# Performance work log

Measured on AMD Instinct MI355X. Metric: run time of the kernel, lower is better.

## Reference

```python
import jax, jax.numpy as jnp
import numpy as np

KTAPS = 10  # kernel_size in StructuredStateSpace.compute_cauchy_kernel


def setup_inputs() -> dict:
    key = jax.random.key(0)
    ks = jax.random.split(key, 6)
    T, B, F, L, OUT = 8192, 16, 32, 16, 128
    return {
        "x": jax.random.normal(ks[0], (T, B, F), dtype=jnp.float32),
        # K[l, s] = C_l @ A_l^s @ B_l, each an (F, F) matrix (in_features == hidden_size)
        "K": jax.random.normal(ks[1], (L, KTAPS, F, F), dtype=jnp.float32),
        # emission_layer[l]: nn.Linear(hidden_size, 1) -> weight (F,), bias scalar per l
        "em_w": jax.random.normal(ks[2], (L, F), dtype=jnp.float32),
        "em_b": jax.random.normal(ks[3], (L,), dtype=jnp.float32),
        # linear_decoder: nn.Linear(L, out_features)
        "dec_w": jax.random.normal(ks[4], (OUT, L), dtype=jnp.float32),
        "dec_b": jax.random.normal(ks[5], (OUT,), dtype=jnp.float32),
    }


def reference(x, K, em_w, em_b, dec_w, dec_b):
    # x: (T, B, F); K: (L, KTAPS, F, F)
    T, B, F = x.shape
    # causal conv: y[l, t] = sum_{s=0}^{min(t, KTAPS-1)} K[l, s] @ x[t - s]
    xp = jnp.pad(x, ((KTAPS - 1, 0), (0, 0), (0, 0)))  # (T+9, B, F)
    # X[s, t] = x[t - s]  -> (KTAPS, T, B, F); loop is over the fixed 10 taps only
    X = jnp.stack([xp[KTAPS - 1 - s:KTAPS - 1 - s + T] for s in range(KTAPS)], axis=0)
    y = jnp.einsum('lsof,stbf->ltbo', K, X)  # (L, T, B, F)
    # per-branch emission Linear(F, 1), stacked over L -> (T, B, L)
    h = jnp.einsum('ltbo,lo->tbl', y, em_w) + em_b
    h = jnp.swapaxes(h, 0, 1)  # (B, T, L)
    # linear_decoder: (B, T, L) -> (B, T, out_features)
    return h @ dec_w.T + dec_b
```

## Files before the change

### kernel.cpp

```cpp
#include <hip/hip_runtime.h>
#include <hip/hip_bf16.h>

typedef __attribute__((ext_vector_type(4))) float f32x4;
typedef __attribute__((ext_vector_type(8))) short bf16x8;

#define T_DIM 8192
#define B_DIM 16
#define F_DIM 32
#define L_DIM 16
#define NTAPS 10
#define O_DIM 128
#define M_TOTAL (T_DIM * B_DIM)

static __device__ __forceinline__ unsigned short f2bf(float f) {
    union { float f; unsigned int u; } v; v.f = f;
    unsigned int r = v.u + 0x7fffu + ((v.u >> 16) & 1u);
    return (unsigned short)(r >> 16);
}

__global__ __launch_bounds__(256) void build_w2_kernel(
    const float* __restrict__ K, const float* __restrict__ em_w,
    const float* __restrict__ em_b, const float* __restrict__ dec_w,
    const float* __restrict__ dec_b, unsigned short* __restrict__ w2f,
    float* __restrict__ bias2)
{
    int s    = blockIdx.x >> 3;
    int nt   = blockIdx.x & 7;
    int lg   = threadIdx.x >> 6;
    int lane = threadIdx.x & 63;
    int o     = nt * 16 + (lane & 15);
    int fbase = (lane >> 4) * 8;

    float acc[8] = {0.f,0.f,0.f,0.f,0.f,0.f,0.f,0.f};
    for (int l = lg * 4; l < lg * 4 + 4; ++l) {
        float dw = dec_w[o * L_DIM + l];
        const float* Kb = K + (size_t)(l * NTAPS + s) * F_DIM * F_DIM;
        for (int op = 0; op < F_DIM; ++op) {
            float e = em_w[l * F_DIM + op] * dw;
            const float* Kr = Kb + op * F_DIM + fbase;
            #pragma unroll
            for (int j = 0; j < 8; ++j) acc[j] += e * Kr[j];
        }
    }

    __shared__ float red[4][64][8];
    #pragma unroll
    for (int j = 0; j < 8; ++j) red[lg][lane][j] = acc[j];
    __syncthreads();

    if (lg == 0) {
        unsigned short out8[8];
        #pragma unroll
        for (int j = 0; j < 8; ++j) {
            float v = red[0][lane][j] + red[1][lane][j] +
                      red[2][lane][j] + red[3][lane][j];
            out8[j] = f2bf(v);
        }
        unsigned short* dst = w2f + ((size_t)(s * 8 + nt) * 64 + lane) * 8;
        *(bf16x8*)dst = *(const bf16x8*)out8;

        if (s == 0 && lane < 16) {
            int oo = nt * 16 + lane;
            float bsum = dec_b[oo];
            for (int l = 0; l < L_DIM; ++l) bsum += dec_w[oo * L_DIM + l] * em_b[l];
            bias2[oo] = bsum;
        }
    }
}

__global__ __launch_bounds__(256) void convert_x_kernel(
    const float* __restrict__ x, unsigned short* __restrict__ xb)
{
    size_t i = ((size_t)blockIdx.x * 256 + threadIdx.x) * 8;
    f32x4 a = *(const f32x4*)(x + i);
    f32x4 b = *(const f32x4*)(x + i + 4);
    unsigned short r[8];
    #pragma unroll
    for (int j = 0; j < 4; ++j) r[j]     = f2bf(a[j]);
    #pragma unroll
    for (int j = 0; j < 4; ++j) r[4 + j] = f2bf(b[j]);
    *(bf16x8*)(xb + i) = *(const bf16x8*)r;
}

__global__ __launch_bounds__(256) void s4_main_kernel(
    const unsigned short* __restrict__ xb,
    const unsigned short* __restrict__ w2f,
    const float* __restrict__ bias2,
    float* __restrict__ out)
{
    int wave = threadIdx.x >> 6;
    int lane = threadIdx.x & 63;
    int row0 = (blockIdx.x * 4 + wave) * 32;

    f32x4 acc[2][8];
    #pragma unroll
    for (int mt = 0; mt < 2; ++mt)
        #pragma unroll
        for (int nt = 0; nt < 8; ++nt)
            acc[mt][nt] = (f32x4){0.f, 0.f, 0.f, 0.f};

    int lrow = lane & 15;
    int fofs = (lane >> 4) * 8;

    for (int s = 0; s < NTAPS; ++s) {
        bf16x8 bfrag[8];
        const bf16x8* wp = (const bf16x8*)w2f + (size_t)(s * 8) * 64 + lane;
        #pragma unroll
        for (int nt = 0; nt < 8; ++nt) bfrag[nt] = wp[nt * 64];

        #pragma unroll
        for (int mt = 0; mt < 2; ++mt) {
            int r0 = row0 + mt * 16 - s * 16;
            if (r0 >= 0) {
                bf16x8 afrag = *(const bf16x8*)(xb + (size_t)(r0 + lrow) * F_DIM + fofs);
                #pragma unroll
                for (int nt = 0; nt < 8; ++nt)
                    acc[mt][nt] = __builtin_amdgcn_mfma_f32_16x16x32_bf16(
                        afrag, bfrag[nt], acc[mt][nt], 0, 0, 0);
            }
        }
    }

    int og = lane & 15;
    int rg = (lane >> 4) * 4;
    #pragma unroll
    for (int mt = 0; mt < 2; ++mt) {
        #pragma unroll
        for (int nt = 0; nt < 8; ++nt) {
            int o = nt * 16 + og;
            float bo = bias2[o];
            #pragma unroll
            for (int j = 0; j < 4; ++j) {
                int r = row0 + mt * 16 + rg + j;
                int t = r >> 4;
                int b = r & 15;
                out[((size_t)b * T_DIM + t) * O_DIM + o] = acc[mt][nt][j] + bo;
            }
        }
    }
}

extern "C" void kernel_launch(void* const* d_in, const int* in_sizes, int n_in,
                              void* d_out, int out_size, void* d_ws, size_t ws_size,
                              hipStream_t stream)
{
    const float* x     = (const float*)d_in[0];
    const float* K     = (const float*)d_in[1];
    const float* em_w  = (const float*)d_in[2];
    const float* em_b  = (const float*)d_in[3];
    const float* dec_w = (const float*)d_in[4];
    const float* dec_b = (const float*)d_in[5];
    float* out = (float*)d_out;

    const size_t xb_bytes  = (size_t)M_TOTAL * F_DIM * 2;
    const size_t w2f_bytes = (size_t)NTAPS * 8 * 64 * 8 * 2;
    unsigned short* xb  = (unsigned short*)d_ws;
    unsigned short* w2f = (unsigned short*)((char*)d_ws + xb_bytes);
    float* bias2 = (float*)((char*)d_ws + xb_bytes + w2f_bytes);

    hipLaunchKernelGGL(build_w2_kernel, dim3(80), dim3(256), 0, stream,
                       K, em_w, em_b, dec_w, dec_b, w2f, bias2);
    hipLaunchKernelGGL(convert_x_kernel, dim3(M_TOTAL * F_DIM / (256 * 8)), dim3(256), 0, stream,
                       x, xb);
    hipLaunchKernelGGL(s4_main_kernel, dim3(M_TOTAL / 128), dim3(256), 0, stream,
                       xb, w2f, bias2, out);
}
```

Baseline: 129.6 us.

## Transpose x to batch-major padded layout and vectorize output stores

The conversion kernel now writes x in a (B, T+16, F) bf16 layout with zero padding in front. The main kernel can then process contiguous time rows per batch and drop the causal-boundary branch. MFMA operands are swapped so each lane holds four consecutive output columns, which enables 16-byte coalesced float4 stores in the (B,T,O) output order instead of scattered scalar stores. The weight-folding kernel is restructured to first reduce em_w against K in LDS and then apply dec_w, using 10 blocks instead of 80. The costs are a strided read in the transpose kernel and lower parallelism in the small prep kernel.

```diff
diff --git a/kernel.cpp b/kernel.cpp
--- a/kernel.cpp
+++ b/kernel.cpp
@@ -11,6 +11,7 @@
 #define NTAPS 10
 #define O_DIM 128
 #define M_TOTAL (T_DIM * B_DIM)
+#define PADT (T_DIM + 16)
 
 static __device__ __forceinline__ unsigned short f2bf(float f) {
     union { float f; unsigned int u; } v; v.f = f;
@@ -24,62 +25,83 @@
     const float* __restrict__ dec_b, unsigned short* __restrict__ w2f,
     float* __restrict__ bias2)
 {
-    int s    = blockIdx.x >> 3;
-    int nt   = blockIdx.x & 7;
-    int lg   = threadIdx.x >> 6;
-    int lane = threadIdx.x & 63;
-    int o     = nt * 16 + (lane & 15);
-    int fbase = (lane >> 4) * 8;
+    int s = blockIdx.x;
+    int tid = threadIdx.x;
 
-    float acc[8] = {0.f,0.f,0.f,0.f,0.f,0.f,0.f,0.f};
-    for (int l = lg * 4; l < lg * 4 + 4; ++l) {
-        float dw = dec_w[o * L_DIM + l];
-        const float* Kb = K + (size_t)(l * NTAPS + s) * F_DIM * F_DIM;
-        for (int op = 0; op < F_DIM; ++op) {
-            float e = em_w[l * F_DIM + op] * dw;
-            const float* Kr = Kb + op * F_DIM + fbase;
+    __shared__ float Klds[16 * 1024];
+    __shared__ float Glds[16 * 32];
+
+    #pragma unroll
+    for (int l = 0; l < 16; ++l) {
+        const float* src = K + (size_t)(l * NTAPS + s) * 1024 + tid * 4;
+        *(f32x4*)(Klds + l * 1024 + tid * 4) = *(const f32x4*)src;
+    }
+    __syncthreads();
+
+    #pragma unroll
+    for (int rep = 0; rep < 2; ++rep) {
+        int idx = rep * 256 + tid;
+        int l = idx >> 5, f = idx & 31;
+        const float* em = em_w + l * 32;
+        const float* kb = Klds + l * 1024 + f;
+        float g = 0.f;
+        #pragma unroll
+        for (int op = 0; op < 32; ++op) g += em[op] * kb[op * 32];
+        Glds[idx] = g;
+    }
+    __syncthreads();
+
+    int lane = tid & 63;
+    int w    = tid >> 6;
+    int lo   = lane & 15;
+    int fb   = (lane >> 4) * 8;
+    #pragma unroll
+    for (int h = 0; h < 2; ++h) {
+        int nt = w + h * 4;
+        int o  = nt * 16 + lo;
+        float acc[8] = {0.f,0.f,0.f,0.f,0.f,0.f,0.f,0.f};
+        for (int l = 0; l < 16; ++l) {
+            float dw = dec_w[o * L_DIM + l];
+            const float* g = Glds + l * 32 + fb;
             #pragma unroll
-            for (int j = 0; j < 8; ++j) acc[j] += e * Kr[j];
+            for (int j = 0; j < 8; ++j) acc[j] += dw * g[j];
         }
+        unsigned short o8[8];
+        #pragma unroll
+        for (int j = 0; j < 8; ++j) o8[j] = f2bf(acc[j]);
+        *(bf16x8*)(w2f + ((size_t)(s * 8 + nt) * 64 + lane) * 8) = *(const bf16x8*)o8;
     }
 
-    __shared__ float red[4][64][8];
-    #pragma unroll
-    for (int j = 0; j < 8; ++j) red[lg][lane][j] = acc[j];
-    __syncthreads();
-
-    if (lg == 0) {
-        unsigned short out8[8];
+    if (s == 0 && tid < O_DIM) {
+        float bsum = dec_b[tid];
         #pragma unroll
-        for (int j = 0; j < 8; ++j) {
-            float v = red[0][lane][j] + red[1][lane][j] +
-                      red[2][lane][j] + red[3][lane][j];
-            out8[j] = f2bf(v);
-        }
-        unsigned short* dst = w2f + ((size_t)(s * 8 + nt) * 64 + lane) * 8;
-        *(bf16x8*)dst = *(const bf16x8*)out8;
-
-        if (s == 0 && lane < 16) {
-            int oo = nt * 16 + lane;
-            float bsum = dec_b[oo];
-            for (int l = 0; l < L_DIM; ++l) bsum += dec_w[oo * L_DIM + l] * em_b[l];
-            bias2[oo] = bsum;
-        }
+        for (int l = 0; l < 16; ++l) bsum += dec_w[tid * L_DIM + l] * em_b[l];
+        bias2[tid] = bsum;
     }
 }
 
 __global__ __launch_bounds__(256) void convert_x_kernel(
     const float* __restrict__ x, unsigned short* __restrict__ xb)
 {
-    size_t i = ((size_t)blockIdx.x * 256 + threadIdx.x) * 8;
-    f32x4 a = *(const f32x4*)(x + i);
-    f32x4 b = *(const f32x4*)(x + i + 4);
-    unsigned short r[8];
+    int b = blockIdx.y;
+    int t = blockIdx.x * 256 + threadIdx.x;
+    const float* src = x + ((size_t)t * B_DIM + b) * F_DIM;
+    unsigned short* dst = xb + ((size_t)b * PADT + 16 + t) * F_DIM;
     #pragma unroll
-    for (int j = 0; j < 4; ++j) r[j]     = f2bf(a[j]);
-    #pragma unroll
-    for (int j = 0; j < 4; ++j) r[4 + j] = f2bf(b[j]);
-    *(bf16x8*)(xb + i) = *(const bf16x8*)r;
+    for (int c = 0; c < 4; ++c) {
+        f32x4 a  = *(const f32x4*)(src + c * 8);
+        f32x4 bb = *(const f32x4*)(src + c * 8 + 4);
+        unsigned short r[8];
+        #pragma unroll
+        for (int j = 0; j < 4; ++j) { r[j] = f2bf(a[j]); r[4 + j] = f2bf(bb[j]); }
+        *(bf16x8*)(dst + c * 8) = *(const bf16x8*)r;
+    }
+    if (blockIdx.x == 0 && threadIdx.x < 16) {
+        unsigned short* pz = xb + ((size_t)b * PADT + threadIdx.x) * F_DIM;
+        bf16x8 z = {0,0,0,0,0,0,0,0};
+        #pragma unroll
+        for (int c = 0; c < 4; ++c) *(bf16x8*)(pz + c * 8) = z;
+    }
 }
 
 __global__ __launch_bounds__(256) void s4_main_kernel(
@@ -90,7 +112,13 @@
 {
     int wave = threadIdx.x >> 6;
     int lane = threadIdx.x & 63;
-    int row0 = (blockIdx.x * 4 + wave) * 32;
+    int R  = (blockIdx.x * 4 + wave) * 32;
+    int b  = R >> 13;
+    int t0 = R & (T_DIM - 1);
+    size_t xrow = (size_t)b * PADT + 16 + t0;
+
+    int lo = lane & 15;
+    int fb = (lane >> 4) * 8;
 
     f32x4 acc[2][8];
     #pragma unroll
@@ -99,43 +127,31 @@
         for (int nt = 0; nt < 8; ++nt)
             acc[mt][nt] = (f32x4){0.f, 0.f, 0.f, 0.f};
 
-    int lrow = lane & 15;
-    int fofs = (lane >> 4) * 8;
-
     for (int s = 0; s < NTAPS; ++s) {
-        bf16x8 bfrag[8];
-        const bf16x8* wp = (const bf16x8*)w2f + (size_t)(s * 8) * 64 + lane;
+        bf16x8 wfrag[8];
+        const bf16x8* wp = (const bf16x8*)w2f + (size_t)s * 8 * 64 + lane;
         #pragma unroll
-        for (int nt = 0; nt < 8; ++nt) bfrag[nt] = wp[nt * 64];
+        for (int nt = 0; nt < 8; ++nt) wfrag[nt] = wp[nt * 64];
 
         #pragma unroll
         for (int mt = 0; mt < 2; ++mt) {
-            int r0 = row0 + mt * 16 - s * 16;
-            if (r0 >= 0) {
-                bf16x8 afrag = *(const bf16x8*)(xb + (size_t)(r0 + lrow) * F_DIM + fofs);
-                #pragma unroll
-                for (int nt = 0; nt < 8; ++nt)
-                    acc[mt][nt] = __builtin_amdgcn_mfma_f32_16x16x32_bf16(
-                        afrag, bfrag[nt], acc[mt][nt], 0, 0, 0);
-            }
+            bf16x8 xfrag = *(const bf16x8*)(xb + (xrow + mt * 16 + lo - s) * F_DIM + fb);
+            #pragma unroll
+            for (int nt = 0; nt < 8; ++nt)
+                acc[mt][nt] = __builtin_amdgcn_mfma_f32_16x16x32_bf16(
+                    wfrag[nt], xfrag, acc[mt][nt], 0, 0, 0);
         }
     }
 
-    int og = lane & 15;
-    int rg = (lane >> 4) * 4;
+    int q = lane >> 4;
     #pragma unroll
-    for (int mt = 0; mt < 2; ++mt) {
+    for (int nt = 0; nt < 8; ++nt) {
+        f32x4 bi = *(const f32x4*)(bias2 + nt * 16 + q * 4);
         #pragma unroll
-        for (int nt = 0; nt < 8; ++nt) {
-            int o = nt * 16 + og;
-            float bo = bias2[o];
-            #pragma unroll
-            for (int j = 0; j < 4; ++j) {
-                int r = row0 + mt * 16 + rg + j;
-                int t = r >> 4;
-                int b = r & 15;
-                out[((size_t)b * T_DIM + t) * O_DIM + o] = acc[mt][nt][j] + bo;
-            }
+        for (int mt = 0; mt < 2; ++mt) {
+            size_t r = (size_t)R + mt * 16 + lo;
+            f32x4 v = acc[mt][nt] + bi;
+            *(f32x4*)(out + r * O_DIM + nt * 16 + q * 4) = v;
         }
     }
 }
@@ -152,15 +168,15 @@
     const float* dec_b = (const float*)d_in[5];
     float* out = (float*)d_out;
 
-    const size_t xb_bytes  = (size_t)M_TOTAL * F_DIM * 2;
+    const size_t xb_bytes  = (size_t)B_DIM * PADT * F_DIM * 2;
     const size_t w2f_bytes = (size_t)NTAPS * 8 * 64 * 8 * 2;
     unsigned short* xb  = (unsigned short*)d_ws;
     unsigned short* w2f = (unsigned short*)((char*)d_ws + xb_bytes);
     float* bias2 = (float*)((char*)d_ws + xb_bytes + w2f_bytes);
 
-    hipLaunchKernelGGL(build_w2_kernel, dim3(80), dim3(256), 0, stream,
+    hipLaunchKernelGGL(build_w2_kernel, dim3(NTAPS), dim3(256), 0, stream,
                        K, em_w, em_b, dec_w, dec_b, w2f, bias2);
-    hipLaunchKernelGGL(convert_x_kernel, dim3(M_TOTAL * F_DIM / (256 * 8)), dim3(256), 0, stream,
+    hipLaunchKernelGGL(convert_x_kernel, dim3(T_DIM / 256, B_DIM), dim3(256), 0, stream,
                        x, xb);
     hipLaunchKernelGGL(s4_main_kernel, dim3(M_TOTAL / 128), dim3(256), 0, stream,
                        xb, w2f, bias2, out);
```

After: 122.3 us. -5.7%, faster.
